# Kernel optimization log

Measured on AMD Instinct MI355X. Metric: run time of the kernel, lower is better.

Reference implementation:

```python
import jax, jax.numpy as jnp
import numpy as np


def setup_inputs() -> dict:
    key = jax.random.key(0)
    ks = jax.random.split(key, 8)
    N, E, F_IN, H, OUT = 20000, 320000, 386, 256, 2
    x = jax.random.normal(ks[0], (N, F_IN), dtype=jnp.float32)
    src = jax.random.randint(ks[1], (E,), 0, N)
    dst = jax.random.randint(ks[2], (E,), 0, N)
    W1 = jax.random.normal(ks[3], (F_IN, H), dtype=jnp.float32) / np.sqrt(F_IN)
    b1 = jnp.zeros((H,), dtype=jnp.float32)
    W2 = jax.random.normal(ks[4], (H, OUT), dtype=jnp.float32) / np.sqrt(H)
    b2 = jnp.zeros((OUT,), dtype=jnp.float32)
    return {"x": x, "src": src, "dst": dst, "W1": W1, "b1": b1, "W2": W2, "b2": b2}


def reference(x, src, dst, W1, b1, W2, b2):
    N = x.shape[0]
    # PyG GCNConv: add self-loops, deg from destination (col), sym normalization
    deg = jnp.ones((N,), x.dtype).at[dst].add(1.0)  # self-loop + in-degree
    dis = deg ** -0.5                                # deg^{-1/2}
    edge_norm = dis[src] * dis[dst]                  # [E]
    self_norm = dis * dis                            # [N] (self-loop weight)

    def gcn_conv(h, W, b):
        h = h @ W                                    # [N, F_out] transform first
        msgs = h[src] * edge_norm[:, None]           # [E, F_out] gathered messages
        agg = jax.ops.segment_sum(msgs, dst, num_segments=N)
        agg = agg + h * self_norm[:, None]           # self-loop contribution
        return agg + b

    h = jax.nn.relu(gcn_conv(x, W1, b1))
    out = gcn_conv(h, W2, b2)
    return jnp.tanh(out)
```

## Files before the change

kernel.cpp:

```cpp
#include <hip/hip_runtime.h>
#include <math.h>

typedef _Float16 f16;
typedef _Float16 f16x8 __attribute__((ext_vector_type(8)));
typedef float f32x4 __attribute__((ext_vector_type(4)));

#define FIN 386
#define KP  416
#define HH  256
#define ELLW 64
#define NP  20032

#define GBM 64
#define GBN 128
#define GBK 32
#define LDP 40


__global__ __launch_bounds__(256) void k_prep(
    int* __restrict__ cursor, int N,
    const float* __restrict__ W1, f16* __restrict__ wt,
    const float* __restrict__ x, f16* __restrict__ xh) {
    int i = blockIdx.x * 256 + threadIdx.x;
    if (i < N) cursor[i] = 0;
    if (i < HH * KP) {
        int c = i / KP, k = i - c * KP;
        wt[i] = (k < FIN) ? (f16)W1[(size_t)k * HH + c] : (f16)0.f;
    }
    const int CPR = KP / 8;
    if (i < NP * CPR) {
        int row = i / CPR;
        int k2 = (i - row * CPR) * 8;
        f16x8 t = {};
        if (row < N && k2 < FIN) {
            const float* p = x + (size_t)row * FIN + k2;
            if (k2 + 8 <= FIN) {
                float2 f0 = *(const float2*)(p);
                float2 f1 = *(const float2*)(p + 2);
                float2 f2 = *(const float2*)(p + 4);
                float2 f3 = *(const float2*)(p + 6);
                t[0] = (f16)f0.x; t[1] = (f16)f0.y;
                t[2] = (f16)f1.x; t[3] = (f16)f1.y;
                t[4] = (f16)f2.x; t[5] = (f16)f2.y;
                t[6] = (f16)f3.x; t[7] = (f16)f3.y;
            } else {
                #pragma unroll
                for (int j = 0; j < 8; ++j)
                    t[j] = (k2 + j < FIN) ? (f16)p[j] : (f16)0.f;
            }
        }
        *(f16x8*)(xh + (size_t)row * KP + k2) = t;
    }
}


__global__ __launch_bounds__(256) void k_mid(
    const f16* __restrict__ A, const f16* __restrict__ Bt,
    f16* __restrict__ C, int nbg,
    const int* __restrict__ src, const int* __restrict__ dst,
    int* __restrict__ cursor, int* __restrict__ ell, int E, int nbf) {
    __shared__ f16 As[GBM * LDP];
    __shared__ f16 Bs[GBN * LDP];

    if ((int)blockIdx.x >= nbg) {
        for (int e = ((int)blockIdx.x - nbg) * 256 + threadIdx.x; e < E; e += nbf * 256) {
            int s = src[e], d = dst[e];
            int slot = atomicAdd(&cursor[d], 1);
            if (slot < ELLW) ell[(size_t)d * ELLW + slot] = s;
        }
        return;
    }

    const int gb = blockIdx.x;
    const int bm = (gb >> 1) * GBM;
    const int bn = (gb & 1) * GBN;
    const int tid = threadIdx.x;
    const int w = tid >> 6, l = tid & 63;
    const int wr = (w & 1) * 32;
    const int wc = (w >> 1) * 64;
    const int lrow = l & 15, lslot = l >> 4;
    const int ar = tid >> 2, ap = tid & 3;

    const f16* agp  = A  + (size_t)(bm + ar) * KP + ap * 8;
    const f16* bgp0 = Bt + (size_t)(bn + ar) * KP + ap * 8;
    const f16* bgp1 = bgp0 + (size_t)64 * KP;

    f32x4 acc[2][4] = {};

    f16x8 av  = *(const f16x8*)(agp);
    f16x8 bv0 = *(const f16x8*)(bgp0);
    f16x8 bv1 = *(const f16x8*)(bgp1);

    for (int k0 = 0; k0 < KP; k0 += GBK) {
        *(f16x8*)&As[ar * LDP + ap * 8] = av;
        *(f16x8*)&Bs[ar * LDP + ap * 8] = bv0;
        *(f16x8*)&Bs[(ar + 64) * LDP + ap * 8] = bv1;
        __syncthreads();

        if (k0 + GBK < KP) {
            av  = *(const f16x8*)(agp + k0 + GBK);
            bv0 = *(const f16x8*)(bgp0 + k0 + GBK);
            bv1 = *(const f16x8*)(bgp1 + k0 + GBK);
        }

        f16x8 a0 = *(const f16x8*)&As[(wr + lrow) * LDP + lslot * 8];
        f16x8 a1 = *(const f16x8*)&As[(wr + 16 + lrow) * LDP + lslot * 8];
        #pragma unroll
        for (int ni = 0; ni < 4; ++ni) {
            f16x8 b = *(const f16x8*)&Bs[(wc + ni * 16 + lrow) * LDP + lslot * 8];
            acc[0][ni] = __builtin_amdgcn_mfma_f32_16x16x32_f16(a0, b, acc[0][ni], 0, 0, 0);
            acc[1][ni] = __builtin_amdgcn_mfma_f32_16x16x32_f16(a1, b, acc[1][ni], 0, 0, 0);
        }
        __syncthreads();
    }

    #pragma unroll
    for (int mi = 0; mi < 2; ++mi) {
        #pragma unroll
        for (int r = 0; r < 4; ++r) {
            int row = bm + wr + mi * 16 + lslot * 4 + r;
            #pragma unroll
            for (int ni = 0; ni < 4; ++ni)
                C[(size_t)row * HH + bn + wc + ni * 16 + lrow] = (f16)acc[mi][ni][r];
        }
    }
}


__global__ __launch_bounds__(256) void k_agg1(
    const f16* __restrict__ h1h, const int* __restrict__ ell,
    const int* __restrict__ cursor, const float* __restrict__ b1,
    const float* __restrict__ W2, float* __restrict__ z, int N) {
    const int sl = threadIdx.x & 31;
    const int d = blockIdx.x * 8 + (threadIdx.x >> 5);
    if (d >= N) return;

    const float4* bp = (const float4*)b1 + sl * 2;
    const float4 bb0 = bp[0], bb1 = bp[1];
    const float4* wp = (const float4*)W2 + sl * 4;
    const float4 wv0 = wp[0], wv1 = wp[1], wv2 = wp[2], wv3 = wp[3];

    int cd = cursor[d];
    float dd = rsqrtf((float)(cd + 1));
    int cnt = cd > ELLW ? ELLW : cd;
    const int* erow = ell + (size_t)d * ELLW;

    f16x8 v = ((const f16x8*)(h1h + (size_t)d * HH))[sl];
    float e[8];
    #pragma unroll
    for (int i = 0; i < 8; ++i) e[i] = dd * (float)v[i];

    int j = 0;
    for (; j + 3 < cnt; j += 4) {
        int s0 = erow[j], s1 = erow[j + 1], s2 = erow[j + 2], s3 = erow[j + 3];
        float u0 = rsqrtf((float)(cursor[s0] + 1));
        float u1 = rsqrtf((float)(cursor[s1] + 1));
        float u2 = rsqrtf((float)(cursor[s2] + 1));
        float u3 = rsqrtf((float)(cursor[s3] + 1));
        f16x8 q0 = ((const f16x8*)(h1h + (size_t)s0 * HH))[sl];
        f16x8 q1 = ((const f16x8*)(h1h + (size_t)s1 * HH))[sl];
        f16x8 q2 = ((const f16x8*)(h1h + (size_t)s2 * HH))[sl];
        f16x8 q3 = ((const f16x8*)(h1h + (size_t)s3 * HH))[sl];
        #pragma unroll
        for (int i = 0; i < 8; ++i)
            e[i] += u0 * (float)q0[i] + u1 * (float)q1[i]
                  + u2 * (float)q2[i] + u3 * (float)q3[i];
    }
    for (; j < cnt; ++j) {
        int s0 = erow[j];
        float u0 = rsqrtf((float)(cursor[s0] + 1));
        f16x8 q0 = ((const f16x8*)(h1h + (size_t)s0 * HH))[sl];
        #pragma unroll
        for (int i = 0; i < 8; ++i) e[i] += u0 * (float)q0[i];
    }

    float a[8];
    a[0] = fmaxf(dd * e[0] + bb0.x, 0.0f);
    a[1] = fmaxf(dd * e[1] + bb0.y, 0.0f);
    a[2] = fmaxf(dd * e[2] + bb0.z, 0.0f);
    a[3] = fmaxf(dd * e[3] + bb0.w, 0.0f);
    a[4] = fmaxf(dd * e[4] + bb1.x, 0.0f);
    a[5] = fmaxf(dd * e[5] + bb1.y, 0.0f);
    a[6] = fmaxf(dd * e[6] + bb1.z, 0.0f);
    a[7] = fmaxf(dd * e[7] + bb1.w, 0.0f);

    float p0 = a[0] * wv0.x + a[1] * wv0.z + a[2] * wv1.x + a[3] * wv1.z
             + a[4] * wv2.x + a[5] * wv2.z + a[6] * wv3.x + a[7] * wv3.z;
    float p1 = a[0] * wv0.y + a[1] * wv0.w + a[2] * wv1.y + a[3] * wv1.w
             + a[4] * wv2.y + a[5] * wv2.w + a[6] * wv3.y + a[7] * wv3.w;
    #pragma unroll
    for (int off = 16; off > 0; off >>= 1) {
        p0 += __shfl_down(p0, off, 32);
        p1 += __shfl_down(p1, off, 32);
    }
    if (sl == 0)
        *(float2*)(z + 2 * (size_t)d) = make_float2(p0, p1);
}


__global__ __launch_bounds__(256) void k_agg2(
    const float* __restrict__ z, const int* __restrict__ ell,
    const int* __restrict__ cursor, const float* __restrict__ b2,
    float* __restrict__ out, int N) {
    int d = blockIdx.x * 256 + threadIdx.x;
    if (d >= N) return;
    const float c0 = b2[0], c1 = b2[1];
    int cd = cursor[d];
    float dd = rsqrtf((float)(cd + 1));
    int cnt = cd > ELLW ? ELLW : cd;
    const int* erow = ell + (size_t)d * ELLW;
    float2 zz = *(const float2*)(z + 2 * (size_t)d);
    float e0 = dd * zz.x, e1 = dd * zz.y;
    int j = 0;
    for (; j + 3 < cnt; j += 4) {
        int s0 = erow[j], s1 = erow[j + 1], s2 = erow[j + 2], s3 = erow[j + 3];
        float u0 = rsqrtf((float)(cursor[s0] + 1));
        float u1 = rsqrtf((float)(cursor[s1] + 1));
        float u2 = rsqrtf((float)(cursor[s2] + 1));
        float u3 = rsqrtf((float)(cursor[s3] + 1));
        float2 z0 = *(const float2*)(z + 2 * (size_t)s0);
        float2 z1 = *(const float2*)(z + 2 * (size_t)s1);
        float2 z2 = *(const float2*)(z + 2 * (size_t)s2);
        float2 z3 = *(const float2*)(z + 2 * (size_t)s3);
        e0 += u0 * z0.x + u1 * z1.x + u2 * z2.x + u3 * z3.x;
        e1 += u0 * z0.y + u1 * z1.y + u2 * z2.y + u3 * z3.y;
    }
    for (; j < cnt; ++j) {
        int s = erow[j];
        float u = rsqrtf((float)(cursor[s] + 1));
        float2 zv = *(const float2*)(z + 2 * (size_t)s);
        e0 += u * zv.x;
        e1 += u * zv.y;
    }
    out[d * 2 + 0] = tanhf(dd * e0 + c0);
    out[d * 2 + 1] = tanhf(dd * e1 + c1);
}


extern "C" void kernel_launch(void* const* d_in, const int* in_sizes, int n_in,
                              void* d_out, int out_size, void* d_ws, size_t ws_size,
                              hipStream_t stream) {
    const float* x   = (const float*)d_in[0];
    const int*   src = (const int*)d_in[1];
    const int*   dst = (const int*)d_in[2];
    const float* W1  = (const float*)d_in[3];
    const float* b1  = (const float*)d_in[4];
    const float* W2  = (const float*)d_in[5];
    const float* b2  = (const float*)d_in[6];
    float* out = (float*)d_out;

    const int E = in_sizes[1];
    const int N = in_sizes[0] / FIN;

    char* base = (char*)d_ws;
    size_t off = 0;
    f16* wt     = (f16*)(base + off); off += (size_t)HH * KP * sizeof(f16);
    f16* xh     = (f16*)(base + off); off += (size_t)NP * KP * sizeof(f16);
    f16* h1h    = (f16*)(base + off); off += (size_t)NP * HH * sizeof(f16);
    int* ell    = (int*)(base + off); off += (size_t)N * ELLW * sizeof(int);
    float* z    = (float*)(base + off); off += 2 * (size_t)N * sizeof(float);
    int* cursor = (int*)(base + off); off += (size_t)N * sizeof(int);

    const int T = 256;
    const int CPR = KP / 8;
    int prep_work = NP * CPR;
    const int nbg = (NP / GBM) * (HH / GBN);
    const int nbf = 512;

    k_prep<<<(prep_work + T - 1) / T, T, 0, stream>>>(cursor, N, W1, wt, x, xh);
    k_mid<<<nbg + nbf, T, 0, stream>>>(xh, wt, h1h, nbg, src, dst, cursor, ell, E, nbf);
    k_agg1<<<(N + 7) / 8, T, 0, stream>>>(h1h, ell, cursor, b1, W2, z, N);
    k_agg2<<<(N + T - 1) / T, T, 0, stream>>>(z, ell, cursor, b2, out, N);
}
```

Measured before the change: 72.15 us.

## Load GEMM MFMA operands directly from global memory, dropping LDS staging

```diff
diff --git a/kernel.cpp b/kernel.cpp
--- a/kernel.cpp
+++ b/kernel.cpp
@@ -14,7 +14,6 @@
 #define GBM 64
 #define GBN 128
 #define GBK 32
-#define LDP 40
 
 
 __global__ __launch_bounds__(256) void k_prep(
@@ -59,8 +58,6 @@
     f16* __restrict__ C, int nbg,
     const int* __restrict__ src, const int* __restrict__ dst,
     int* __restrict__ cursor, int* __restrict__ ell, int E, int nbf) {
-    __shared__ f16 As[GBM * LDP];
-    __shared__ f16 Bs[GBN * LDP];
 
     if ((int)blockIdx.x >= nbg) {
         for (int e = ((int)blockIdx.x - nbg) * 256 + threadIdx.x; e < E; e += nbf * 256) {
@@ -79,39 +76,29 @@
     const int wr = (w & 1) * 32;
     const int wc = (w >> 1) * 64;
     const int lrow = l & 15, lslot = l >> 4;
-    const int ar = tid >> 2, ap = tid & 3;
-
-    const f16* agp  = A  + (size_t)(bm + ar) * KP + ap * 8;
-    const f16* bgp0 = Bt + (size_t)(bn + ar) * KP + ap * 8;
-    const f16* bgp1 = bgp0 + (size_t)64 * KP;
+
+    const f16* pa0 = A  + (size_t)(bm + wr + lrow) * KP + lslot * 8;
+    const f16* pa1 = pa0 + (size_t)16 * KP;
+    const f16* pb  = Bt + (size_t)(bn + wc + lrow) * KP + lslot * 8;
 
     f32x4 acc[2][4] = {};
 
-    f16x8 av  = *(const f16x8*)(agp);
-    f16x8 bv0 = *(const f16x8*)(bgp0);
-    f16x8 bv1 = *(const f16x8*)(bgp1);
-
+    #pragma unroll
     for (int k0 = 0; k0 < KP; k0 += GBK) {
-        *(f16x8*)&As[ar * LDP + ap * 8] = av;
-        *(f16x8*)&Bs[ar * LDP + ap * 8] = bv0;
-        *(f16x8*)&Bs[(ar + 64) * LDP + ap * 8] = bv1;
-        __syncthreads();
-
-        if (k0 + GBK < KP) {
-            av  = *(const f16x8*)(agp + k0 + GBK);
-            bv0 = *(const f16x8*)(bgp0 + k0 + GBK);
-            bv1 = *(const f16x8*)(bgp1 + k0 + GBK);
-        }
-
-        f16x8 a0 = *(const f16x8*)&As[(wr + lrow) * LDP + lslot * 8];
-        f16x8 a1 = *(const f16x8*)&As[(wr + 16 + lrow) * LDP + lslot * 8];
-        #pragma unroll
-        for (int ni = 0; ni < 4; ++ni) {
-            f16x8 b = *(const f16x8*)&Bs[(wc + ni * 16 + lrow) * LDP + lslot * 8];
-            acc[0][ni] = __builtin_amdgcn_mfma_f32_16x16x32_f16(a0, b, acc[0][ni], 0, 0, 0);
-            acc[1][ni] = __builtin_amdgcn_mfma_f32_16x16x32_f16(a1, b, acc[1][ni], 0, 0, 0);
-        }
-        __syncthreads();
+        f16x8 a0 = *(const f16x8*)(pa0 + k0);
+        f16x8 a1 = *(const f16x8*)(pa1 + k0);
+        f16x8 b0 = *(const f16x8*)(pb + k0);
+        f16x8 b1 = *(const f16x8*)(pb + (size_t)16 * KP + k0);
+        f16x8 b2 = *(const f16x8*)(pb + (size_t)32 * KP + k0);
+        f16x8 b3 = *(const f16x8*)(pb + (size_t)48 * KP + k0);
+        acc[0][0] = __builtin_amdgcn_mfma_f32_16x16x32_f16(a0, b0, acc[0][0], 0, 0, 0);
+        acc[1][0] = __builtin_amdgcn_mfma_f32_16x16x32_f16(a1, b0, acc[1][0], 0, 0, 0);
+        acc[0][1] = __builtin_amdgcn_mfma_f32_16x16x32_f16(a0, b1, acc[0][1], 0, 0, 0);
+        acc[1][1] = __builtin_amdgcn_mfma_f32_16x16x32_f16(a1, b1, acc[1][1], 0, 0, 0);
+        acc[0][2] = __builtin_amdgcn_mfma_f32_16x16x32_f16(a0, b2, acc[0][2], 0, 0, 0);
+        acc[1][2] = __builtin_amdgcn_mfma_f32_16x16x32_f16(a1, b2, acc[1][2], 0, 0, 0);
+        acc[0][3] = __builtin_amdgcn_mfma_f32_16x16x32_f16(a0, b3, acc[0][3], 0, 0, 0);
+        acc[1][3] = __builtin_amdgcn_mfma_f32_16x16x32_f16(a1, b3, acc[1][3], 0, 0, 0);
     }
 
     #pragma unroll
```

After: 71.64 us, median of 2. Within noise of the previous version (-0.7%).
